# Kernel optimization log

Measured on AMD Instinct MI355X. Metric: run time of the kernel, lower is better.

## Reference

```python
import jax, jax.numpy as jnp
import numpy as np
from jax import lax

K = 5  # kernel size
PAD = (K - 1) // 2


def setup_inputs() -> dict:
    key = jax.random.key(0)
    k1, k2, k3 = jax.random.split(key, 3)
    B, C, H, W = 16, 3, 256, 256
    x = jax.random.normal(k1, (B, C, H, W), dtype=jnp.float32)
    # Conv2d(3 -> 25, kernel=5) params, PyTorch-style fan-in init scale
    fan_in = C * K * K
    bound = 1.0 / np.sqrt(fan_in)
    conv_w = jax.random.uniform(k2, (K * K, C, K, K), dtype=jnp.float32, minval=-bound, maxval=bound)
    conv_b = jax.random.uniform(k3, (K * K,), dtype=jnp.float32, minval=-bound, maxval=bound)
    return {"x": x, "conv_w": conv_w, "conv_b": conv_b}


def reference(x, conv_w, conv_b):
    B, C, H, W = x.shape
    # weights = conv(x): [B, 25, H, W], one scalar weight per tap per pixel
    w = lax.conv_general_dilated(
        x, conv_w, window_strides=(1, 1), padding=((PAD, PAD), (PAD, PAD)),
        dimension_numbers=("NCHW", "OIHW", "NCHW"),
    ) + conv_b[None, :, None, None]
    # dynamic per-pixel 5x5 weighted neighborhood aggregation (zero-padded)
    xp = jnp.pad(x, ((0, 0), (0, 0), (PAD, PAD), (PAD, PAD)))
    out = jnp.zeros_like(x)
    k = 0
    for i in range(K):
        for j in range(K):
            # w[:, k] broadcasts over channels; xp slice is the (i,j)-shifted input
            out = out + w[:, k:k + 1] * xp[:, :, i:i + H, j:j + W]
            k += 1
    return out + x  # residual
```

## Files before the change

kernel.cpp:

```cpp
#include <hip/hip_runtime.h>
#include <stdint.h>

typedef __fp16    half2v __attribute__((ext_vector_type(2)));
typedef _Float16  f16x8  __attribute__((ext_vector_type(8)));
typedef float     f32x4  __attribute__((ext_vector_type(4)));
typedef uint32_t  u32x4  __attribute__((ext_vector_type(4)));

#define KSZ    5
#define NBATCH 16
#define NC     3
#define NH     256
#define NW     256
#define TW     16
#define TH     16
#define NTAP   25
#define TROWS  20
#define TWRD   12
#define CPLANE (TROWS * TWRD)
#define COPYW  (NC * CPLANE)
#define PTS    20

__device__ __forceinline__ uint32_t pack_f16x2(float lo, float hi) {
    half2v h = __builtin_amdgcn_cvt_pkrtz(lo, hi);
    return __builtin_bit_cast(uint32_t, h);
}

__device__ __forceinline__ float fdot2(uint32_t w, uint32_t v, float acc) {
#if __has_builtin(__builtin_amdgcn_fdot2)
    return __builtin_amdgcn_fdot2(__builtin_bit_cast(half2v, w),
                                  __builtin_bit_cast(half2v, v), acc, false);
#else
    half2v a = __builtin_bit_cast(half2v, w);
    half2v b = __builtin_bit_cast(half2v, v);
    return acc + (float)a.x * (float)b.x + (float)a.y * (float)b.y;
#endif
}

__device__ __forceinline__ int pair_of(int s, int d) {
    return (d < 2) ? (2 * s + d) : (8 + 2 * s + (d - 2));
}

__global__ void prep_AB(const float* __restrict__ cw, const float* __restrict__ cb,
                        uint32_t* __restrict__ Atab, float* __restrict__ cbv)
{
    int idx = threadIdx.x + blockIdx.x * 256;
    if (idx < 1536) {
        int d  = idx & 3;
        int fl = (idx >> 2) & 15;
        int s  = (idx >> 6) & 3;
        int t3 = idx >> 8;
        int c  = t3 % 3, mt = t3 / 3;
        int vf = mt * 16 + fl;
        int P  = pair_of(s, d);
        float lo = 0.0f, hi = 0.0f;
        if (vf < 30 && (vf % 6) != 5 && P < 15) {
            int f = (vf / 6) * 5 + (vf % 6);
            int i = P / 3, q = P - 3 * i;
            const float* base = cw + f * 75 + c * 25 + i * 5;
            lo = base[2 * q];
            if (q < 2) hi = base[2 * q + 1];
        }
        Atab[idx] = pack_f16x2(lo, hi);
    } else if (idx < 1568) {
        int vf = idx - 1536;
        float v = 0.0f;
        if (vf < 30 && (vf % 6) != 5) v = cb[(vf / 6) * 5 + (vf % 6)];
        cbv[vf] = v;
    }
}

__global__ __launch_bounds__(256, 4)
void highorder13(const float* __restrict__ x,
                 const uint32_t* __restrict__ Atab,
                 const float* __restrict__ cbv,
                 float* __restrict__ out)
{
    __shared__ uint32_t lds_t[2 * COPYW];
    __shared__ uint32_t pbuf[TH * 16 * PTS];

    const int tid = threadIdx.x;
    const int l   = tid & 63;
    const int w   = tid >> 6;
    const int fl  = l & 15;
    const int s   = l >> 4;

    const int bx  = blockIdx.x & 15;
    const int by  = (blockIdx.x >> 4) & 15;
    const int b   = blockIdx.x >> 8;
    const int bw0 = bx * TW;
    const int bh0 = by * TH;

    const float* xb = x + (size_t)b * NC * NH * NW;

    u32x4 afr[6];
    const u32x4* At4 = (const u32x4*)Atab;
    #pragma unroll
    for (int t3 = 0; t3 < 6; ++t3)
        afr[t3] = At4[(t3 * 4 + s) * 16 + fl];
    const f32x4* cbv4 = (const f32x4*)cbv;
    const f32x4 cbA = cbv4[s];
    const f32x4 cbB = cbv4[4 + s];

    #pragma unroll
    for (int it = 0; it < 3; ++it) {
        int idx = tid + it * 256;
        if (idx < COPYW) {
            int c   = idx / CPLANE;
            int rem = idx - c * CPLANE;
            int r   = rem / TWRD;
            int m   = rem - r * TWRD;
            int gh  = bh0 + r - 2;
            int g0  = bw0 + 2 * m - 2;
            bool rowok = (unsigned)gh < NH;
            const float* row = xb + c * NH * NW + gh * NW;
            float a0 = (rowok && (unsigned)(g0)     < NW) ? row[g0]     : 0.0f;
            float a1 = (rowok && (unsigned)(g0 + 1) < NW) ? row[g0 + 1] : 0.0f;
            float a2 = (rowok && (unsigned)(g0 + 2) < NW) ? row[g0 + 2] : 0.0f;
            lds_t[idx]         = pack_f16x2(a0, a1);
            lds_t[COPYW + idx] = pack_f16x2(a1, a2);
        }
    }
    __syncthreads();

    int woff[4];
    #pragma unroll
    for (int d = 0; d < 4; ++d) {
        int P = pair_of(s, d);
        int i = P / 3, q = P - 3 * i;
        woff[d] = (P == 15) ? 0 : (i * TWRD + q);
    }
    const int abase = ((fl & 1) ? COPYW : 0) + (fl >> 1);

    #pragma unroll
    for (int g = 0; g < 4; ++g) {
        const int py = w * 4 + g;
        const int bg = abase + py * TWRD;

        u32x4 bv[3];
        #pragma unroll
        for (int c = 0; c < 3; ++c)
            #pragma unroll
            for (int d = 0; d < 4; ++d)
                bv[c][d] = lds_t[bg + c * CPLANE + woff[d]];

        f32x4 a0 = cbA, a1 = cbB;
        #pragma unroll
        for (int c = 0; c < 3; ++c) {
            f16x8 B = __builtin_bit_cast(f16x8, bv[c]);
            a0 = __builtin_amdgcn_mfma_f32_16x16x32_f16(
                     __builtin_bit_cast(f16x8, afr[c]),     B, a0, 0, 0, 0);
            a1 = __builtin_amdgcn_mfma_f32_16x16x32_f16(
                     __builtin_bit_cast(f16x8, afr[3 + c]), B, a1, 0, 0, 0);
        }

        uint32_t wq0 = pack_f16x2(a0[0], a0[1]);
        uint32_t wq1 = pack_f16x2(a0[2], a0[3]);
        uint32_t wq2 = pack_f16x2(a1[0], a1[1]);
        uint32_t wq3 = pack_f16x2(a1[2], a1[3]);

        const int pb = (py * 16 + fl) * PTS;
        uint2 w01; w01.x = wq0; w01.y = wq1;
        uint2 w23; w23.x = wq2; w23.y = wq3;
        *reinterpret_cast<uint2*>(&pbuf[pb + 2 * s])     = w01;
        *reinterpret_cast<uint2*>(&pbuf[pb + 8 + 2 * s]) = w23;
    }

    const int px  = tid & 15;
    const int py2 = tid >> 4;
    const uint32_t* basep = lds_t + ((px & 1) ? COPYW : 0) + (px >> 1);

    uint32_t nb[45];
    #pragma unroll
    for (int c = 0; c < NC; ++c)
        #pragma unroll
        for (int i = 0; i < KSZ; ++i)
            #pragma unroll
            for (int q = 0; q < 3; ++q)
                nb[c * 15 + i * 3 + q] =
                    basep[c * CPLANE + (py2 + i) * TWRD + q];

    __syncthreads();

    u32x4 wp4[4];
    const int rb = (py2 * 16 + px) * PTS;
    #pragma unroll
    for (int r = 0; r < 4; ++r)
        wp4[r] = *reinterpret_cast<const u32x4*>(&pbuf[rb + 4 * r]);

    float* ob = out + (size_t)b * NC * NH * NW
                    + (size_t)(bh0 + py2) * NW + (bw0 + px);
    #pragma unroll
    for (int c = 0; c < NC; ++c) {
        half2v ctr = __builtin_bit_cast(half2v, nb[c * 15 + 7]);
        float sumA = (float)ctr.x;
        float sumB = 0.0f;
        #pragma unroll
        for (int t = 0; t < 8; ++t)
            sumA = fdot2(wp4[t >> 2][t & 3], nb[c * 15 + t], sumA);
        #pragma unroll
        for (int t = 8; t < 15; ++t)
            sumB = fdot2(wp4[t >> 2][t & 3], nb[c * 15 + t], sumB);
        ob[(size_t)c * NH * NW] = sumA + sumB;
    }
}

extern "C" void kernel_launch(void* const* d_in, const int* in_sizes, int n_in,
                              void* d_out, int out_size, void* d_ws, size_t ws_size,
                              hipStream_t stream)
{
    const float* x  = (const float*)d_in[0];
    const float* cw = (const float*)d_in[1];
    const float* cb = (const float*)d_in[2];
    float* out      = (float*)d_out;
    uint32_t* Atab  = (uint32_t*)d_ws;
    float*    cbv   = (float*)((char*)d_ws + 6144);

    prep_AB<<<7, 256, 0, stream>>>(cw, cb, Atab, cbv);

    dim3 grid(NBATCH * (NH / TH) * (NW / TW));
    highorder13<<<grid, 256, 0, stream>>>(x, Atab, cbv, out);
}
```

Measured before the change: 27.94 us.

## Process four batch images per block with double-buffered LDS prefetch

Each block now loops over four batch images for the same spatial tile. The next image's halo is loaded from global memory into registers while the current one runs its MFMA and dot-product work, then written into the alternate LDS buffer. Tile loading also switches to 4-wide vector loads with a fast path for interior tiles. This amortizes the A-fragment and bias setup and hides global latency, but the grid shrinks to a quarter of the blocks, and the larger LDS and register footprint may cut occupancy.

```diff
diff --git a/kernel.cpp b/kernel.cpp
--- a/kernel.cpp
+++ b/kernel.cpp
@@ -13,12 +13,13 @@
 #define NW     256
 #define TW     16
 #define TH     16
-#define NTAP   25
 #define TROWS  20
 #define TWRD   12
 #define CPLANE (TROWS * TWRD)
 #define COPYW  (NC * CPLANE)
 #define PTS    20
+#define NUNIT  (COPYW / 2)
+#define TB     4
 
 __device__ __forceinline__ uint32_t pack_f16x2(float lo, float hi) {
     half2v h = __builtin_amdgcn_cvt_pkrtz(lo, hi);
@@ -70,12 +71,12 @@
 }
 
 __global__ __launch_bounds__(256, 4)
-void highorder13(const float* __restrict__ x,
+void highorder18(const float* __restrict__ x,
                  const uint32_t* __restrict__ Atab,
                  const float* __restrict__ cbv,
                  float* __restrict__ out)
 {
-    __shared__ uint32_t lds_t[2 * COPYW];
+    __shared__ uint32_t lds_t[2][2 * COPYW];
     __shared__ uint32_t pbuf[TH * 16 * PTS];
 
     const int tid = threadIdx.x;
@@ -86,11 +87,11 @@
 
     const int bx  = blockIdx.x & 15;
     const int by  = (blockIdx.x >> 4) & 15;
-    const int b   = blockIdx.x >> 8;
+    const int bb  = blockIdx.x >> 8;
+    const int b0  = bb * TB;
     const int bw0 = bx * TW;
     const int bh0 = by * TH;
-
-    const float* xb = x + (size_t)b * NC * NH * NW;
+    const size_t bstride = (size_t)NC * NH * NW;
 
     u32x4 afr[6];
     const u32x4* At4 = (const u32x4*)Atab;
@@ -101,24 +102,55 @@
     const f32x4 cbA = cbv4[s];
     const f32x4 cbB = cbv4[4 + s];
 
-    #pragma unroll
-    for (int it = 0; it < 3; ++it) {
-        int idx = tid + it * 256;
-        if (idx < COPYW) {
-            int c   = idx / CPLANE;
-            int rem = idx - c * CPLANE;
-            int r   = rem / TWRD;
-            int m   = rem - r * TWRD;
-            int gh  = bh0 + r - 2;
-            int g0  = bw0 + 2 * m - 2;
-            bool rowok = (unsigned)gh < NH;
-            const float* row = xb + c * NH * NW + gh * NW;
-            float a0 = (rowok && (unsigned)(g0)     < NW) ? row[g0]     : 0.0f;
-            float a1 = (rowok && (unsigned)(g0 + 1) < NW) ? row[g0 + 1] : 0.0f;
-            float a2 = (rowok && (unsigned)(g0 + 2) < NW) ? row[g0 + 2] : 0.0f;
-            lds_t[idx]         = pack_f16x2(a0, a1);
-            lds_t[COPYW + idx] = pack_f16x2(a1, a2);
-        }
+    int  uoff[2], ug0[2], uidx[2];
+    bool uval[2], urok[2], ufast[2];
+    #pragma unroll
+    for (int e = 0; e < 2; ++e) {
+        int u   = tid + e * 256;
+        uval[e] = (u < NUNIT);
+        int uu  = uval[e] ? u : 0;
+        int c   = uu / 120;
+        int rem = uu - c * 120;
+        int r   = rem / 6;
+        int j   = rem - r * 6;
+        int gh  = bh0 + r - 2;
+        int g0  = bw0 + 4 * j - 2;
+        bool rowok = (unsigned)gh < NH;
+        urok[e]  = rowok;
+        ufast[e] = rowok && g0 >= 0 && g0 + 4 < NW;
+        uoff[e]  = c * NH * NW + (rowok ? gh : 0) * NW;
+        ug0[e]   = g0;
+        uidx[e]  = 2 * uu;
+    }
+
+    auto ldu = [&](const float* xb, int e, float v[5]) {
+        const float* row = xb + uoff[e];
+        const int g0 = ug0[e];
+        if (ufast[e]) {
+            f32x4 t = *reinterpret_cast<const f32x4*>(row + g0);
+            v[0] = t[0]; v[1] = t[1]; v[2] = t[2]; v[3] = t[3];
+            v[4] = row[g0 + 4];
+        } else {
+            bool rk = urok[e];
+            v[0] = (rk && (unsigned)(g0)     < NW) ? row[g0]     : 0.0f;
+            v[1] = (rk && (unsigned)(g0 + 1) < NW) ? row[g0 + 1] : 0.0f;
+            v[2] = (rk && (unsigned)(g0 + 2) < NW) ? row[g0 + 2] : 0.0f;
+            v[3] = (rk && (unsigned)(g0 + 3) < NW) ? row[g0 + 3] : 0.0f;
+            v[4] = (rk && (unsigned)(g0 + 4) < NW) ? row[g0 + 4] : 0.0f;
+        }
+    };
+    auto wru = [&](uint32_t* buf, int e, const float v[5]) {
+        uint2 wa; wa.x = pack_f16x2(v[0], v[1]); wa.y = pack_f16x2(v[2], v[3]);
+        uint2 wb; wb.x = pack_f16x2(v[1], v[2]); wb.y = pack_f16x2(v[3], v[4]);
+        *reinterpret_cast<uint2*>(&buf[uidx[e]])         = wa;
+        *reinterpret_cast<uint2*>(&buf[COPYW + uidx[e]]) = wb;
+    };
+
+    {
+        const float* xb0 = x + (size_t)b0 * bstride;
+        #pragma unroll
+        for (int e = 0; e < 2; ++e)
+            if (uval[e]) { float v[5]; ldu(xb0, e, v); wru(lds_t[0], e, v); }
     }
     __syncthreads();
 
@@ -130,77 +162,96 @@
         woff[d] = (P == 15) ? 0 : (i * TWRD + q);
     }
     const int abase = ((fl & 1) ? COPYW : 0) + (fl >> 1);
-
-    #pragma unroll
-    for (int g = 0; g < 4; ++g) {
-        const int py = w * 4 + g;
-        const int bg = abase + py * TWRD;
-
-        u32x4 bv[3];
-        #pragma unroll
-        for (int c = 0; c < 3; ++c)
-            #pragma unroll
-            for (int d = 0; d < 4; ++d)
-                bv[c][d] = lds_t[bg + c * CPLANE + woff[d]];
-
-        f32x4 a0 = cbA, a1 = cbB;
-        #pragma unroll
-        for (int c = 0; c < 3; ++c) {
-            f16x8 B = __builtin_bit_cast(f16x8, bv[c]);
-            a0 = __builtin_amdgcn_mfma_f32_16x16x32_f16(
-                     __builtin_bit_cast(f16x8, afr[c]),     B, a0, 0, 0, 0);
-            a1 = __builtin_amdgcn_mfma_f32_16x16x32_f16(
-                     __builtin_bit_cast(f16x8, afr[3 + c]), B, a1, 0, 0, 0);
-        }
-
-        uint32_t wq0 = pack_f16x2(a0[0], a0[1]);
-        uint32_t wq1 = pack_f16x2(a0[2], a0[3]);
-        uint32_t wq2 = pack_f16x2(a1[0], a1[1]);
-        uint32_t wq3 = pack_f16x2(a1[2], a1[3]);
-
-        const int pb = (py * 16 + fl) * PTS;
-        uint2 w01; w01.x = wq0; w01.y = wq1;
-        uint2 w23; w23.x = wq2; w23.y = wq3;
-        *reinterpret_cast<uint2*>(&pbuf[pb + 2 * s])     = w01;
-        *reinterpret_cast<uint2*>(&pbuf[pb + 8 + 2 * s]) = w23;
-    }
-
     const int px  = tid & 15;
     const int py2 = tid >> 4;
-    const uint32_t* basep = lds_t + ((px & 1) ? COPYW : 0) + (px >> 1);
-
-    uint32_t nb[45];
-    #pragma unroll
-    for (int c = 0; c < NC; ++c)
-        #pragma unroll
-        for (int i = 0; i < KSZ; ++i)
-            #pragma unroll
-            for (int q = 0; q < 3; ++q)
-                nb[c * 15 + i * 3 + q] =
-                    basep[c * CPLANE + (py2 + i) * TWRD + q];
-
-    __syncthreads();
-
-    u32x4 wp4[4];
-    const int rb = (py2 * 16 + px) * PTS;
-    #pragma unroll
-    for (int r = 0; r < 4; ++r)
-        wp4[r] = *reinterpret_cast<const u32x4*>(&pbuf[rb + 4 * r]);
-
-    float* ob = out + (size_t)b * NC * NH * NW
-                    + (size_t)(bh0 + py2) * NW + (bw0 + px);
-    #pragma unroll
-    for (int c = 0; c < NC; ++c) {
-        half2v ctr = __builtin_bit_cast(half2v, nb[c * 15 + 7]);
-        float sumA = (float)ctr.x;
-        float sumB = 0.0f;
-        #pragma unroll
-        for (int t = 0; t < 8; ++t)
-            sumA = fdot2(wp4[t >> 2][t & 3], nb[c * 15 + t], sumA);
-        #pragma unroll
-        for (int t = 8; t < 15; ++t)
-            sumB = fdot2(wp4[t >> 2][t & 3], nb[c * 15 + t], sumB);
-        ob[(size_t)c * NH * NW] = sumA + sumB;
+    const int rb  = (py2 * 16 + px) * PTS;
+
+    #pragma unroll
+    for (int k = 0; k < TB; ++k) {
+        const int cur = k & 1;
+        const uint32_t* tb = lds_t[cur];
+
+        float nx0[5], nx1[5];
+        if (k < TB - 1) {
+            const float* xbn = x + (size_t)(b0 + k + 1) * bstride;
+            if (uval[0]) ldu(xbn, 0, nx0);
+            if (uval[1]) ldu(xbn, 1, nx1);
+        }
+
+        #pragma unroll
+        for (int g = 0; g < 4; ++g) {
+            const int py = w * 4 + g;
+            const int bg = abase + py * TWRD;
+
+            u32x4 bv[3];
+            #pragma unroll
+            for (int c = 0; c < 3; ++c)
+                #pragma unroll
+                for (int d = 0; d < 4; ++d)
+                    bv[c][d] = tb[bg + c * CPLANE + woff[d]];
+
+            f32x4 a0 = cbA, a1 = cbB;
+            #pragma unroll
+            for (int c = 0; c < 3; ++c) {
+                f16x8 B = __builtin_bit_cast(f16x8, bv[c]);
+                a0 = __builtin_amdgcn_mfma_f32_16x16x32_f16(
+                         __builtin_bit_cast(f16x8, afr[c]),     B, a0, 0, 0, 0);
+                a1 = __builtin_amdgcn_mfma_f32_16x16x32_f16(
+                         __builtin_bit_cast(f16x8, afr[3 + c]), B, a1, 0, 0, 0);
+            }
+
+            uint32_t wq0 = pack_f16x2(a0[0], a0[1]);
+            uint32_t wq1 = pack_f16x2(a0[2], a0[3]);
+            uint32_t wq2 = pack_f16x2(a1[0], a1[1]);
+            uint32_t wq3 = pack_f16x2(a1[2], a1[3]);
+
+            const int pb = (py * 16 + fl) * PTS;
+            uint2 w01; w01.x = wq0; w01.y = wq1;
+            uint2 w23; w23.x = wq2; w23.y = wq3;
+            *reinterpret_cast<uint2*>(&pbuf[pb + 2 * s])     = w01;
+            *reinterpret_cast<uint2*>(&pbuf[pb + 8 + 2 * s]) = w23;
+        }
+
+        const uint32_t* basep = tb + ((px & 1) ? COPYW : 0) + (px >> 1);
+        uint32_t nb[45];
+        #pragma unroll
+        for (int c = 0; c < NC; ++c)
+            #pragma unroll
+            for (int i = 0; i < KSZ; ++i)
+                #pragma unroll
+                for (int q = 0; q < 3; ++q)
+                    nb[c * 15 + i * 3 + q] =
+                        basep[c * CPLANE + (py2 + i) * TWRD + q];
+
+        __syncthreads();
+
+        if (k < TB - 1) {
+            if (uval[0]) wru(lds_t[cur ^ 1], 0, nx0);
+            if (uval[1]) wru(lds_t[cur ^ 1], 1, nx1);
+        }
+
+        u32x4 wp4[4];
+        #pragma unroll
+        for (int r = 0; r < 4; ++r)
+            wp4[r] = *reinterpret_cast<const u32x4*>(&pbuf[rb + 4 * r]);
+
+        float* ob = out + (size_t)(b0 + k) * bstride
+                        + (size_t)(bh0 + py2) * NW + (bw0 + px);
+        #pragma unroll
+        for (int c = 0; c < NC; ++c) {
+            half2v ctr = __builtin_bit_cast(half2v, nb[c * 15 + 7]);
+            float sumA = (float)ctr.x;
+            float sumB = 0.0f;
+            #pragma unroll
+            for (int t = 0; t < 8; ++t)
+                sumA = fdot2(wp4[t >> 2][t & 3], nb[c * 15 + t], sumA);
+            #pragma unroll
+            for (int t = 8; t < 15; ++t)
+                sumB = fdot2(wp4[t >> 2][t & 3], nb[c * 15 + t], sumB);
+            ob[(size_t)c * NH * NW] = sumA + sumB;
+        }
+
+        if (k < TB - 1) __syncthreads();
     }
 }
 
@@ -217,6 +268,6 @@
 
     prep_AB<<<7, 256, 0, stream>>>(cw, cb, Atab, cbv);
 
-    dim3 grid(NBATCH * (NH / TH) * (NW / TW));
-    highorder13<<<grid, 256, 0, stream>>>(x, Atab, cbv, out);
-}
+    dim3 grid((NH / TH) * (NW / TW) * (NBATCH / TB));
+    highorder18<<<grid, 256, 0, stream>>>(x, Atab, cbv, out);
+}
```

Measured after the change: 42.50 us. +52.1%, slower.
